# Performance work log

Hardware: AMD Instinct MI355X
Metric: run time of the kernel (lower is better)

The kernel has to match this reference:

```python
import jax, jax.numpy as jnp
import numpy as np

N_GRAPHS = 100
NODES_PER_GRAPH = 1000
N = N_GRAPHS * NODES_PER_GRAPH
DEG = 16
E = N * DEG
IN_FEATS = 64
HIDDEN = 128
READOUT_DIM = HIDDEN // 2
SLOPE = 0.01
EPS = 1e-5


def leaky(x):
    return jnp.where(x >= 0, x, SLOPE * x)


def _kaiming(k, shape):
    # torch kaiming_uniform_, fan_in mode, leaky_relu gain
    fan_in = shape[0]
    gain = np.sqrt(2.0 / (1.0 + SLOPE ** 2))
    bound = gain * np.sqrt(3.0 / fan_in)
    return jax.random.uniform(k, shape, jnp.float32, -bound, bound)


def setup_inputs() -> dict:
    key = jax.random.key(0)
    ks = jax.random.split(key, 16)
    node_feats = jax.random.normal(ks[0], (N, IN_FEATS), jnp.float32)
    # within-graph random edges (batched graph of equal-sized components)
    src_local = jax.random.randint(ks[1], (E,), 0, NODES_PER_GRAPH)
    dst_local = jax.random.randint(ks[2], (E,), 0, NODES_PER_GRAPH)
    edge_graph = jnp.repeat(jnp.arange(N_GRAPHS, dtype=jnp.int32), E // N_GRAPHS)
    src = (edge_graph * NODES_PER_GRAPH + src_local).astype(jnp.int32)
    dst = (edge_graph * NODES_PER_GRAPH + dst_local).astype(jnp.int32)
    edge_weights = jax.random.uniform(ks[3], (E,), jnp.float32)
    node_graph = jnp.repeat(jnp.arange(N_GRAPHS, dtype=jnp.int32), NODES_PER_GRAPH)
    return {
        "node_feats": node_feats,
        "edge_weights": edge_weights,
        "W1": _kaiming(ks[4], (IN_FEATS, HIDDEN)),
        "W2": _kaiming(ks[5], (HIDDEN, HIDDEN)),
        "gn1_alpha": jnp.ones((HIDDEN,), jnp.float32),
        "gn1_gamma": jnp.ones((HIDDEN,), jnp.float32),
        "gn1_beta": jnp.zeros((HIDDEN,), jnp.float32),
        "gn2_alpha": jnp.ones((HIDDEN,), jnp.float32),
        "gn2_gamma": jnp.ones((HIDDEN,), jnp.float32),
        "gn2_beta": jnp.zeros((HIDDEN,), jnp.float32),
        "r1_w1": _kaiming(ks[6], (HIDDEN, HIDDEN)),
        "r1_b1": jnp.zeros((HIDDEN,), jnp.float32),
        "r1_w2": _kaiming(ks[7], (HIDDEN, READOUT_DIM)),
        "r1_b2": jnp.zeros((READOUT_DIM,), jnp.float32),
        "r2_w1": _kaiming(ks[8], (HIDDEN, HIDDEN)),
        "r2_b1": jnp.zeros((HIDDEN,), jnp.float32),
        "r2_w2": _kaiming(ks[9], (HIDDEN, READOUT_DIM)),
        "r2_b2": jnp.zeros((READOUT_DIM,), jnp.float32),
        "src": src,
        "dst": dst,
        "node_graph": node_graph,
    }


def _graph_conv(x, W, src, dst, ew, out_isqrt, in_isqrt):
    # DGL GraphConv norm='both', no bias: D_in^{-1/2} A_w D_out^{-1/2} X W
    h = (x * out_isqrt[:, None]) @ W                 # [N, out]
    m = h[src] * ew[:, None]                         # [E, out] gather + edge weight
    agg = jax.ops.segment_sum(m, dst, num_segments=N)  # scatter-add
    return agg * in_isqrt[:, None]


def _graph_norm(x, alpha, gamma, beta, node_graph, inv_cnt):
    mean = jax.ops.segment_sum(x, node_graph, num_segments=N_GRAPHS) * inv_cnt
    sub = x - alpha * mean[node_graph]
    var = jax.ops.segment_sum(sub * sub, node_graph, num_segments=N_GRAPHS) * inv_cnt
    return gamma * sub / jnp.sqrt(var[node_graph] + EPS) + beta


def _readout(x, w1, b1, w2, b2, node_graph, inv_cnt):
    # deep-sets style universal readout: rho(mean(phi(h_v)))
    h = leaky(x @ w1 + b1)
    pooled = jax.ops.segment_sum(h, node_graph, num_segments=N_GRAPHS) * inv_cnt
    return leaky(pooled @ w2 + b2)


def reference(node_feats, edge_weights, W1, W2,
              gn1_alpha, gn1_gamma, gn1_beta,
              gn2_alpha, gn2_gamma, gn2_beta,
              r1_w1, r1_b1, r1_w2, r1_b2,
              r2_w1, r2_b1, r2_w2, r2_b2,
              src, dst, node_graph):
    ones_e = jnp.ones((E,), jnp.float32)
    out_deg = jnp.clip(jax.ops.segment_sum(ones_e, src, num_segments=N), 1.0)
    in_deg = jnp.clip(jax.ops.segment_sum(ones_e, dst, num_segments=N), 1.0)
    out_isqrt = jax.lax.rsqrt(out_deg)
    in_isqrt = jax.lax.rsqrt(in_deg)
    inv_cnt = 1.0 / NODES_PER_GRAPH

    h = _graph_conv(node_feats, W1, src, dst, edge_weights, out_isqrt, in_isqrt)
    h = leaky(_graph_norm(h, gn1_alpha, gn1_gamma, gn1_beta, node_graph, inv_cnt))
    # dropout is identity in eval mode
    r1 = _readout(h, r1_w1, r1_b1, r1_w2, r1_b2, node_graph, inv_cnt)
    m1 = jax.ops.segment_sum(h, node_graph, num_segments=N_GRAPHS) * inv_cnt

    h = _graph_conv(h, W2, src, dst, edge_weights, out_isqrt, in_isqrt)
    h = leaky(_graph_norm(h, gn2_alpha, gn2_gamma, gn2_beta, node_graph, inv_cnt))
    r2 = _readout(h, r2_w1, r2_b1, r2_w2, r2_b2, node_graph, inv_cnt)
    m2 = jax.ops.segment_sum(h, node_graph, num_segments=N_GRAPHS) * inv_cnt

    readout = jnp.concatenate([r1, m1, r2, m2], axis=1)  # [G, 2*H + 2*H/2] = [100, 384]
    return leaky(readout)
```

## Files before the change

### kernel.cpp

```cpp
#include <hip/hip_runtime.h>
#include <cstddef>
#include <cstdint>

#define NG   100
#define NPG  1000
#define NN   (NG * NPG)
#define NE   (NN * 16)
#define EPG  (NE / NG)
#define CSRL 24000
#define MINREC 20
#define FIN  64
#define HID  128
#define RD   64
#define SLOPE 0.01f
#define EPSV  1e-5f
#define NSTRIP 500
#define GSN   40

using short8 = __attribute__((ext_vector_type(8))) short;
using f32x4  = __attribute__((ext_vector_type(4))) float;
typedef unsigned short u16;

__device__ __forceinline__ float leaky(float x) { return x >= 0.f ? x : SLOPE * x; }

__device__ __forceinline__ u16 f2bf(float f) {
  union { float f; unsigned u; } v; v.f = f;
  return (u16)((v.u + 0x7fffu + ((v.u >> 16) & 1u)) >> 16);
}
__device__ __forceinline__ float bf2f(u16 u) {
  union { unsigned u; float f; } v; v.u = ((unsigned)u) << 16;
  return v.f;
}

__device__ __forceinline__ bool swz(int b, int per_g, int& g, int& part) {
  const int xcd = b & 7;
  const int slot = b >> 3;
  g = xcd + 8 * (slot / per_g);
  part = slot % per_g;
  return g < NG;
}

struct BldSh {
  unsigned csrl[CSRL];
  int hin[NPG];
  int hout[NPG];
  int cur[NPG];
  int wtot[16];
  int total;
};
struct GemSh { u16 Xl[64 * FIN]; u16 W[HID * FIN]; };
union FrontSh { BldSh b; GemSh g; };

__global__ __launch_bounds__(1024) void front_k(
    const float* __restrict__ X0, const float* __restrict__ ew,
    const int* __restrict__ src, const int* __restrict__ dst,
    const float* __restrict__ W1, const float* __restrict__ W2f,
    const float* __restrict__ R1f, const float* __restrict__ R2f,
    u16* __restrict__ Wt2, u16* __restrict__ Rt1, u16* __restrict__ Rt2,
    int* __restrict__ cin_, int* __restrict__ offs,
    unsigned* __restrict__ csr, u16* __restrict__ bufA,
    float* __restrict__ zeroreg) {
  __shared__ FrontSh u;
  const int b = blockIdx.x;
  const int t = threadIdx.x;
  if (b >= 208) {
    const int idx = (b - 208) * 1024 + t;
    {
      const int m = idx >> 14, r = idx & 16383;
      const int n = r >> 7, k = r & 127;
      const float* s = (m == 0) ? W2f : (m == 1) ? R1f : R2f;
      u16* d = (m == 0) ? Wt2 : (m == 1) ? Rt1 : Rt2;
      d[r] = f2bf(s[k * HID + n]);
    }
    if (idx < (8 * NG * HID) / 4)
      ((float4*)zeroreg)[idx] = make_float4(0.f, 0.f, 0.f, 0.f);
    return;
  }
  int g, part;
  if (!swz(b, 2, g, part)) return;
  const int lane = t & 63, wave = t >> 6;
  const int nb = g * NPG, eb = g * EPG;

  if (part == 0) {
    {
      const uint4 z4 = {0u, 0u, 0u, 0u};
      uint4* c4 = (uint4*)u.b.csrl;
#pragma unroll
      for (int i = 0; i < CSRL / 4 / 1024 + 1; ++i) {
        const int j = t + i * 1024;
        if (j < CSRL / 4) c4[j] = z4;
      }
    }
    if (t < NPG) { u.b.hin[t] = 0; u.b.hout[t] = 0; }
    __syncthreads();
    for (int e = t; e < EPG; e += 4096) {
      int s4[4], d4[4];
#pragma unroll
      for (int k = 0; k < 4; ++k) {
        const int ee = e + k * 1024;
        if (ee < EPG) { s4[k] = src[eb + ee]; d4[k] = dst[eb + ee]; }
        else d4[k] = -1;
      }
#pragma unroll
      for (int k = 0; k < 4; ++k)
        if (d4[k] >= 0) {
          atomicAdd(&u.b.hout[s4[k] - nb], 1);
          atomicAdd(&u.b.hin[d4[k] - nb], 1);
        }
    }
    __syncthreads();
    int v[4], vr[4];
    int loc = 0;
#pragma unroll
    for (int k = 0; k < 4; ++k) {
      const int idx = t * 4 + k;
      v[k] = (idx < NPG) ? u.b.hin[idx] : 0;
      const int c4 = (v[k] + 3) & ~3;
      vr[k] = (idx < NPG) ? ((c4 > MINREC) ? c4 : MINREC) : 0;
      loc += vr[k];
    }
    int incl = loc;
#pragma unroll
    for (int d = 1; d < 64; d <<= 1) {
      const int x = __shfl_up(incl, d);
      if (lane >= d) incl += x;
    }
    if (lane == 63) u.b.wtot[wave] = incl;
    if (t < NPG) cin_[nb + t] = u.b.hin[t];
    __syncthreads();
    float* houtf = (float*)u.b.hout;
    if (t < NPG) {
      const int c = u.b.hout[t];
      houtf[t] = rsqrtf((float)(c > 0 ? c : 1));
    }
    int wexc = 0;
    for (int i = 0; i < wave; ++i) wexc += u.b.wtot[i];
    int run = wexc + (incl - loc);
#pragma unroll
    for (int k = 0; k < 4; ++k) {
      const int idx = t * 4 + k;
      if (idx < NPG) {
        offs[nb + idx] = g * CSRL + run;
        u.b.cur[idx] = run;
        run += vr[k];
        if (idx == NPG - 1) u.b.total = run;
      }
    }
    __syncthreads();
    for (int e = t; e < EPG; e += 4096) {
      int s4[4], d4[4];
      float w4[4];
#pragma unroll
      for (int k = 0; k < 4; ++k) {
        const int ee = e + k * 1024;
        if (ee < EPG) { s4[k] = src[eb + ee]; d4[k] = dst[eb + ee]; w4[k] = ew[eb + ee]; }
        else d4[k] = -1;
      }
#pragma unroll
      for (int k = 0; k < 4; ++k)
        if (d4[k] >= 0) {
          const int sl = s4[k] - nb;
          const int pos = atomicAdd(&u.b.cur[d4[k] - nb], 1);
          if (pos < CSRL)
            u.b.csrl[pos] = ((unsigned)sl << 16) | (unsigned)f2bf(w4[k] * houtf[sl]);
        }
    }
    __syncthreads();
    {
      const int tot4 = (u.b.total + 3) >> 2;
      const uint4* s4p = (const uint4*)u.b.csrl;
      uint4* d4p = (uint4*)(csr + (size_t)g * CSRL);
      for (int i = t; i < tot4; i += 1024) d4p[i] = s4p[i];
    }
  } else {
    const int l15 = lane & 15, quad = lane >> 4;
    const int rg = wave >> 2, cg = wave & 3;
    {
      const int n = t & 127, ko = t >> 7;
      short8 w8;
#pragma unroll
      for (int j = 0; j < 8; ++j) w8[j] = (short)f2bf(W1[(ko * 8 + j) * HID + n]);
      *(short8*)&u.g.W[n * FIN + ((ko ^ (n & 7)) << 3)] = w8;
    }
    const int kq = t & 15, srow = t >> 4;
    float4 xpre = (srow < NPG)
        ? *(const float4*)(X0 + (size_t)(nb + srow) * FIN + kq * 4)
        : make_float4(0.f, 0.f, 0.f, 0.f);
    for (int pass = 0; pass < 16; ++pass) {
      __syncthreads();
      {
        ushort4 uu = make_ushort4(f2bf(xpre.x), f2bf(xpre.y), f2bf(xpre.z), f2bf(xpre.w));
        const int cc = kq >> 1, half = kq & 1;
        *(ushort4*)&u.g.Xl[srow * FIN + (((cc ^ (srow & 7)) << 3) | (half << 2))] = uu;
      }
      __syncthreads();
      if (pass < 15) {
        const int rowi = (pass + 1) * 64 + srow;
        xpre = (rowi < NPG)
            ? *(const float4*)(X0 + (size_t)(nb + rowi) * FIN + kq * 4)
            : make_float4(0.f, 0.f, 0.f, 0.f);
      }
      short8 a[2];
      const int arow = rg * 16 + l15;
#pragma unroll
      for (int kt = 0; kt < 2; ++kt)
        a[kt] = *(const short8*)&u.g.Xl[arow * FIN + (((kt * 4 + quad) ^ (l15 & 7)) << 3)];
      int rows[4];
#pragma unroll
      for (int r = 0; r < 4; ++r) rows[r] = pass * 64 + rg * 16 + quad * 4 + r;
#pragma unroll
      for (int q2 = 0; q2 < 2; ++q2) {
        const int ct = cg * 2 + q2;
        f32x4 acc = {0.f, 0.f, 0.f, 0.f};
        const int brow = ct * 16 + l15;
#pragma unroll
        for (int kt = 0; kt < 2; ++kt) {
          const short8 bb = *(const short8*)&u.g.W[brow * FIN + (((kt * 4 + quad) ^ (l15 & 7)) << 3)];
          acc = __builtin_amdgcn_mfma_f32_16x16x32_bf16(a[kt], bb, acc, 0, 0, 0);
        }
        const int n2 = ct * 16 + l15;
#pragma unroll
        for (int r = 0; r < 4; ++r)
          if (rows[r] < NPG)
            bufA[(size_t)(nb + rows[r]) * HID + n2] = f2bf(acc[r]);
      }
    }
  }
}

__device__ __forceinline__ void norm_affine(const float* sx, const float* sq,
                                            const float* alpha, const float* gamma,
                                            const float* beta, int g, int c8,
                                            float* Av, float* Bv) {
  const float inv = 1.0f / NPG;
#pragma unroll
  for (int j = 0; j < 8; ++j) {
    const int f = c8 * 8 + j;
    const float mean = sx[g * HID + f] * inv;
    const float ex2 = sq[g * HID + f] * inv;
    const float am = alpha[f] * mean;
    const float var = fmaxf(ex2 - 2.0f * am * mean + am * am, 0.0f);
    const float A = gamma[f] * rsqrtf(var + EPSV);
    Av[j] = A;
    Bv[j] = beta[f] - A * am;
  }
}

__global__ __launch_bounds__(256) void gather_k(const u16* __restrict__ H,
                                                const unsigned* __restrict__ csr,
                                                const int* __restrict__ offs,
                                                const int* __restrict__ cin_,
                                                u16* __restrict__ AGG,
                                                float* __restrict__ sx,
                                                float* __restrict__ sq) {
  __shared__ float redx[4][HID];
  __shared__ float redq[4][HID];
  const int wave = threadIdx.x >> 6;
  const int lane = threadIdx.x & 63;
  int g, part;
  if (!swz(blockIdx.x, 25, g, part)) return;
  const int nb = g * NPG;
  const int base = nb + part * GSN;
  const int loff = lane * 2;
  const u16* __restrict__ Hg = H + (size_t)nb * HID;

  float sxa = 0.f, sxb = 0.f, sqa = 0.f, sqb = 0.f;
  for (int it = 0; it < 3; ++it) {
    const int nc = (it < 2) ? 4 : 2;
    int nn[4], cnt[4], c4p[4];
    float isq[4];
    const uint4* p[4];
#pragma unroll
    for (int c = 0; c < 4; ++c) {
      const int j = it * 4 + c;
      const int node = base + wave + ((j < 10) ? j : 0) * 4;
      nn[c] = node;
      const int nu = __builtin_amdgcn_readfirstlane(node);
      const int off = __builtin_amdgcn_readfirstlane(offs[nu]);
      cnt[c] = (c < nc) ? __builtin_amdgcn_readfirstlane(cin_[nu]) : 0;
      const int cr = (cnt[c] + 3) & ~3;
      c4p[c] = ((cr > MINREC) ? cr : MINREC) >> 2;
      isq[c] = rsqrtf(fmaxf((float)cnt[c], 1.0f));
      p[c] = (const uint4*)__builtin_assume_aligned(csr + off, 16);
    }
    float ax[4] = {0.f, 0.f, 0.f, 0.f};
    float ay[4] = {0.f, 0.f, 0.f, 0.f};
#pragma unroll
    for (int t = 0; t < 5; ++t) {
      unsigned rs[4][4];
#pragma unroll
      for (int c = 0; c < 4; ++c)
        if (c < nc) {
          const uint4 rv = p[c][t];
          rs[c][0] = __builtin_amdgcn_readfirstlane(rv.x);
          rs[c][1] = __builtin_amdgcn_readfirstlane(rv.y);
          rs[c][2] = __builtin_amdgcn_readfirstlane(rv.z);
          rs[c][3] = __builtin_amdgcn_readfirstlane(rv.w);
        }
      unsigned uu[4][4];
#pragma unroll
      for (int c = 0; c < 4; ++c)
        if (c < nc) {
#pragma unroll
          for (int q = 0; q < 4; ++q)
            uu[c][q] = ((const unsigned*)(Hg + (size_t)(rs[c][q] >> 16) * HID))[lane];
        }
#pragma unroll
      for (int c = 0; c < 4; ++c)
        if (c < nc) {
#pragma unroll
          for (int q = 0; q < 4; ++q) {
            const float w = bf2f((u16)(rs[c][q] & 0xffffu));
            ax[c] = fmaf(w, __uint_as_float(uu[c][q] << 16), ax[c]);
            ay[c] = fmaf(w, __uint_as_float(uu[c][q] & 0xffff0000u), ay[c]);
          }
        }
    }
#pragma unroll
    for (int c = 0; c < 4; ++c) {
      for (int t = 5; t < c4p[c]; ++t) {
        const uint4 rv = p[c][t];
        unsigned rsd[4];
        rsd[0] = __builtin_amdgcn_readfirstlane(rv.x);
        rsd[1] = __builtin_amdgcn_readfirstlane(rv.y);
        rsd[2] = __builtin_amdgcn_readfirstlane(rv.z);
        rsd[3] = __builtin_amdgcn_readfirstlane(rv.w);
#pragma unroll
        for (int q = 0; q < 4; ++q) {
          const unsigned uq = ((const unsigned*)(Hg + (size_t)(rsd[q] >> 16) * HID))[lane];
          const float w = bf2f((u16)(rsd[q] & 0xffffu));
          ax[c] = fmaf(w, __uint_as_float(uq << 16), ax[c]);
          ay[c] = fmaf(w, __uint_as_float(uq & 0xffff0000u), ay[c]);
        }
      }
    }
#pragma unroll
    for (int c = 0; c < 4; ++c)
      if (c < nc) {
        const float rx = ax[c] * isq[c];
        const float ry = ay[c] * isq[c];
        *(unsigned*)(AGG + (size_t)nn[c] * HID + loff) =
            (unsigned)f2bf(rx) | ((unsigned)f2bf(ry) << 16);
        sxa += rx; sxb += ry;
        sqa += rx * rx; sqb += ry * ry;
      }
  }
  redx[wave][loff] = sxa; redx[wave][loff + 1] = sxb;
  redq[wave][loff] = sqa; redq[wave][loff + 1] = sqb;
  __syncthreads();
  const int tid = threadIdx.x;
  if (tid < HID) {
    unsafeAtomicAdd(&sx[g * HID + tid],
                    redx[0][tid] + redx[1][tid] + redx[2][tid] + redx[3][tid]);
  } else {
    const int t = tid - HID;
    unsafeAtomicAdd(&sq[g * HID + t],
                    redq[0][t] + redq[1][t] + redq[2][t] + redq[3][t]);
  }
}

struct RedT { float red[32][HID]; float hred[32][HID]; };
union ShT { u16 Xl[128 * HID]; RedT r; };

template <bool DO_GEMM>
__global__ __launch_bounds__(512) void phigemm_k(const u16* __restrict__ Xb,
                                                 u16* __restrict__ Y,
                                                 const u16* __restrict__ Wt,
                                                 const u16* __restrict__ Rt,
                                                 const float* __restrict__ sx,
                                                 const float* __restrict__ sq,
                                                 const float* __restrict__ alpha,
                                                 const float* __restrict__ gamma,
                                                 const float* __restrict__ beta,
                                                 const float* __restrict__ b1,
                                                 float* __restrict__ phi_sum,
                                                 float* __restrict__ h_sum) {
  __shared__ ShT sh;
  __shared__ u16 Rl[HID * HID];
  __shared__ u16 Wl[DO_GEMM ? HID * HID : 8];
  const int tid = threadIdx.x;
  const int wave = tid >> 6, lane = tid & 63, l15 = lane & 15, quad = lane >> 4;
  int g, part;
  if (!swz(blockIdx.x, 2, g, part)) return;
  const int base = g * NPG + part * NSTRIP;
  const int c8 = tid & 15;
  const int srow = tid >> 4;

  for (int i = tid; i < HID * (HID / 8); i += 512) {
    const int n = i >> 4, c = i & 15;
    const short8 r2 = *(const short8*)(Rt + n * HID + c * 8);
    *(short8*)&Rl[n * HID + ((c ^ (n & 15)) << 3)] = r2;
    if (DO_GEMM) {
      const short8 w = *(const short8*)(Wt + n * HID + c * 8);
      *(short8*)&Wl[n * HID + ((c ^ (n & 15)) << 3)] = w;
    }
  }
  float Av[8], Bv[8];
  norm_affine(sx, sq, alpha, gamma, beta, g, c8, Av, Bv);
  float bcol[8];
#pragma unroll
  for (int ct = 0; ct < 8; ++ct) bcol[ct] = b1[ct * 16 + l15];

  float pooled[8] = {0.f, 0.f, 0.f, 0.f, 0.f, 0.f, 0.f, 0.f};
  float hp[8] = {0.f, 0.f, 0.f, 0.f, 0.f, 0.f, 0.f, 0.f};
  const short8 z8 = {0, 0, 0, 0, 0, 0, 0, 0};
  short8 xpre[4];
#pragma unroll
  for (int it = 0; it < 4; ++it) {
    const int rowi = srow + it * 32;
    xpre[it] = (rowi < NSTRIP) ? *(const short8*)(Xb + (size_t)(base + rowi) * HID + c8 * 8) : z8;
  }
  for (int pass = 0; pass < 4; ++pass) {
    __syncthreads();
#pragma unroll
    for (int it = 0; it < 4; ++it) {
      const int r = srow + it * 32;
      const int rowi = pass * 128 + r;
      short8 o = z8;
      if (rowi < NSTRIP) {
#pragma unroll
        for (int j = 0; j < 8; ++j) {
          const float xn = leaky(fmaf(Av[j], bf2f((u16)xpre[it][j]), Bv[j]));
          hp[j] += xn;
          o[j] = (short)f2bf(xn);
        }
      }
      *(short8*)&sh.Xl[r * HID + ((c8 ^ (r & 15)) << 3)] = o;
    }
    __syncthreads();
    if (pass < 3) {
#pragma unroll
      for (int it = 0; it < 4; ++it) {
        const int rowi = (pass + 1) * 128 + srow + it * 32;
        xpre[it] = (rowi < NSTRIP) ? *(const short8*)(Xb + (size_t)(base + rowi) * HID + c8 * 8) : z8;
      }
    }
    short8 a[4];
    const int arow = wave * 16 + l15;
#pragma unroll
    for (int kt = 0; kt < 4; ++kt)
      a[kt] = *(const short8*)&sh.Xl[arow * HID + (((kt * 4 + quad) ^ l15) << 3)];
    int rows[4];
#pragma unroll
    for (int r = 0; r < 4; ++r) rows[r] = pass * 128 + wave * 16 + quad * 4 + r;
#pragma unroll
    for (int ct = 0; ct < 8; ++ct) {
      const int brow = ct * 16 + l15;
      if (DO_GEMM) {
        f32x4 accW = {0.f, 0.f, 0.f, 0.f};
#pragma unroll
        for (int kt = 0; kt < 4; ++kt) {
          const short8 bb = *(const short8*)&Wl[brow * HID + (((kt * 4 + quad) ^ l15) << 3)];
          accW = __builtin_amdgcn_mfma_f32_16x16x32_bf16(a[kt], bb, accW, 0, 0, 0);
        }
#pragma unroll
        for (int r = 0; r < 4; ++r)
          if (rows[r] < NSTRIP)
            Y[(size_t)(base + rows[r]) * HID + ct * 16 + l15] = f2bf(accW[r]);
      }
      f32x4 accR = {0.f, 0.f, 0.f, 0.f};
#pragma unroll
      for (int kt = 0; kt < 4; ++kt) {
        const short8 bb = *(const short8*)&Rl[brow * HID + (((kt * 4 + quad) ^ l15) << 3)];
        accR = __builtin_amdgcn_mfma_f32_16x16x32_bf16(a[kt], bb, accR, 0, 0, 0);
      }
#pragma unroll
      for (int r = 0; r < 4; ++r)
        if (rows[r] < NSTRIP) pooled[ct] += leaky(accR[r] + bcol[ct]);
    }
  }
  __syncthreads();
  const int qi = wave * 4 + quad;
#pragma unroll
  for (int ct = 0; ct < 8; ++ct) sh.r.red[qi][ct * 16 + l15] = pooled[ct];
#pragma unroll
  for (int j = 0; j < 8; ++j) sh.r.hred[tid >> 4][(tid & 15) * 8 + j] = hp[j];
  __syncthreads();
  if (tid < HID) {
    float s = 0.f;
#pragma unroll
    for (int q = 0; q < 32; ++q) s += sh.r.red[q][tid];
    unsafeAtomicAdd(&phi_sum[g * HID + tid], s);
  } else if (tid < 2 * HID) {
    const int t = tid - HID;
    float s = 0.f;
#pragma unroll
    for (int rr = 0; rr < 32; ++rr) s += sh.r.hred[rr][t];
    unsafeAtomicAdd(&h_sum[g * HID + t], s);
  }
}

__global__ __launch_bounds__(64) void fin_k(const float* __restrict__ ps1,
                                            const float* __restrict__ hs1,
                                            const float* __restrict__ ps2,
                                            const float* __restrict__ hs2,
                                            const float* __restrict__ r1w2,
                                            const float* __restrict__ r1b2,
                                            const float* __restrict__ r2w2,
                                            const float* __restrict__ r2b2,
                                            float* __restrict__ out) {
  const int gb = blockIdx.x;
  const bool L2 = gb >= NG;
  const int g = L2 ? gb - NG : gb;
  const float* ps = L2 ? ps2 : ps1;
  const float* hs = L2 ? hs2 : hs1;
  const float* w2 = L2 ? r2w2 : r1w2;
  const float* b2 = L2 ? r2b2 : r1b2;
  const int roff = L2 ? 192 : 0;
  const int moff = L2 ? 256 : 64;
  const int j = threadIdx.x;
  float acc = b2[j];
#pragma unroll 8
  for (int k = 0; k < HID; ++k)
    acc += (ps[g * HID + k] * (1.0f / NPG)) * w2[k * RD + j];
  out[g * 384 + roff + j] = leaky(leaky(acc));
  out[g * 384 + moff + j] = leaky(hs[g * HID + j] * (1.0f / NPG));
  out[g * 384 + moff + 64 + j] = leaky(hs[g * HID + 64 + j] * (1.0f / NPG));
}

extern "C" void kernel_launch(void* const* d_in, const int* in_sizes, int n_in,
                              void* d_out, int out_size, void* d_ws, size_t ws_size,
                              hipStream_t stream) {
  const float* node_feats = (const float*)d_in[0];
  const float* ew   = (const float*)d_in[1];
  const float* W1   = (const float*)d_in[2];
  const float* W2   = (const float*)d_in[3];
  const float* g1a  = (const float*)d_in[4];
  const float* g1g  = (const float*)d_in[5];
  const float* g1b  = (const float*)d_in[6];
  const float* g2a  = (const float*)d_in[7];
  const float* g2g  = (const float*)d_in[8];
  const float* g2b  = (const float*)d_in[9];
  const float* r1w1 = (const float*)d_in[10];
  const float* r1b1 = (const float*)d_in[11];
  const float* r1w2 = (const float*)d_in[12];
  const float* r1b2 = (const float*)d_in[13];
  const float* r2w1 = (const float*)d_in[14];
  const float* r2b1 = (const float*)d_in[15];
  const float* r2w2 = (const float*)d_in[16];
  const float* r2b2 = (const float*)d_in[17];
  const int* src = (const int*)d_in[18];
  const int* dst = (const int*)d_in[19];
  float* out = (float*)d_out;

  char* wsb = (char*)d_ws;
  float* ps1     = (float*)wsb;
  float* hs1     = ps1 + NG * HID;
  float* ps2     = hs1 + NG * HID;
  float* hs2     = ps2 + NG * HID;
  float* sx1     = hs2 + NG * HID;
  float* sq1     = sx1 + NG * HID;
  float* sx2     = sq1 + NG * HID;
  float* sq2     = sx2 + NG * HID;
  int*   cin     = (int*)(sq2 + NG * HID);
  int*   offs    = cin + NN;
  unsigned* csr  = (unsigned*)(offs + NN);
  u16*   Wt2     = (u16*)(csr + (size_t)NG * CSRL);
  u16*   Rt1     = Wt2 + HID * HID;
  u16*   Rt2     = Rt1 + HID * HID;
  u16*   bufA    = Rt2 + HID * HID;
  u16*   bufB    = bufA + (size_t)NN * HID;

  const int gemm_grid = 8 * 2 * 13;
  const int gather_grid = 8 * 25 * 13;

  front_k<<<256, 1024, 0, stream>>>(node_feats, ew, src, dst,
                                    W1, W2, r1w1, r2w1,
                                    Wt2, Rt1, Rt2,
                                    cin, offs, csr, bufA, ps1);

  gather_k<<<gather_grid, 256, 0, stream>>>(bufA, csr, offs, cin, bufB, sx1, sq1);
  phigemm_k<true><<<gemm_grid, 512, 0, stream>>>(bufB, bufA, Wt2, Rt1,
                                                 sx1, sq1, g1a, g1g, g1b,
                                                 r1b1, ps1, hs1);

  gather_k<<<gather_grid, 256, 0, stream>>>(bufA, csr, offs, cin, bufB, sx2, sq2);
  phigemm_k<false><<<gemm_grid, 512, 0, stream>>>(bufB, nullptr, nullptr, Rt2,
                                                  sx2, sq2, g2a, g2g, g2b,
                                                  r2b1, ps2, hs2);

  fin_k<<<2 * NG, 64, 0, stream>>>(ps1, hs1, ps2, hs2, r1w2, r1b2, r2w2, r2b2, out);
}
```

Baseline: 257.5 us.

## Split per-graph CSR build across two blocks by destination half

The per-graph CSR construction in the front kernel is now split across two blocks, each owning 500 destination nodes, with its own half-size shared CSR buffer and offset base. The grid grows to 3 parts per graph (two build, one GEMM) so build work runs in parallel and shared memory per block shrinks, which can improve occupancy. Each build block still scans all edges of the graph and recomputes the out-degree histogram, so edge loads and histogram work are duplicated.

```diff
diff --git a/kernel.cpp b/kernel.cpp
--- a/kernel.cpp
+++ b/kernel.cpp
@@ -8,6 +8,7 @@
 #define NE   (NN * 16)
 #define EPG  (NE / NG)
 #define CSRL 24000
+#define CSRH 12000
 #define MINREC 20
 #define FIN  64
 #define HID  128
@@ -41,11 +42,11 @@
 }
 
 struct BldSh {
-  unsigned csrl[CSRL];
-  int hin[NPG];
+  unsigned csrl[CSRH];
   int hout[NPG];
-  int cur[NPG];
-  int wtot[16];
+  int hin[NPG / 2];
+  int cur[NPG / 2];
+  int wtot[8];
   int total;
 };
 struct GemSh { u16 Xl[64 * FIN]; u16 W[HID * FIN]; };
@@ -63,8 +64,8 @@
   __shared__ FrontSh u;
   const int b = blockIdx.x;
   const int t = threadIdx.x;
-  if (b >= 208) {
-    const int idx = (b - 208) * 1024 + t;
+  if (b >= 312) {
+    const int idx = (b - 312) * 1024 + t;
     {
       const int m = idx >> 14, r = idx & 16383;
       const int n = r >> 7, k = r & 127;
@@ -77,21 +78,23 @@
     return;
   }
   int g, part;
-  if (!swz(b, 2, g, part)) return;
+  if (!swz(b, 3, g, part)) return;
   const int lane = t & 63, wave = t >> 6;
   const int nb = g * NPG, eb = g * EPG;
 
-  if (part == 0) {
+  if (part < 2) {
+    const int nbase = part * 500;
     {
       const uint4 z4 = {0u, 0u, 0u, 0u};
       uint4* c4 = (uint4*)u.b.csrl;
 #pragma unroll
-      for (int i = 0; i < CSRL / 4 / 1024 + 1; ++i) {
+      for (int i = 0; i < 3; ++i) {
         const int j = t + i * 1024;
-        if (j < CSRL / 4) c4[j] = z4;
-      }
-    }
-    if (t < NPG) { u.b.hin[t] = 0; u.b.hout[t] = 0; }
+        if (j < CSRH / 4) c4[j] = z4;
+      }
+    }
+    if (t < NPG) u.b.hout[t] = 0;
+    if (t < 500) u.b.hin[t] = 0;
     __syncthreads();
     for (int e = t; e < EPG; e += 4096) {
       int s4[4], d4[4];
@@ -105,46 +108,39 @@
       for (int k = 0; k < 4; ++k)
         if (d4[k] >= 0) {
           atomicAdd(&u.b.hout[s4[k] - nb], 1);
-          atomicAdd(&u.b.hin[d4[k] - nb], 1);
-        }
-    }
-    __syncthreads();
-    int v[4], vr[4];
-    int loc = 0;
-#pragma unroll
-    for (int k = 0; k < 4; ++k) {
-      const int idx = t * 4 + k;
-      v[k] = (idx < NPG) ? u.b.hin[idx] : 0;
-      const int c4 = (v[k] + 3) & ~3;
-      vr[k] = (idx < NPG) ? ((c4 > MINREC) ? c4 : MINREC) : 0;
-      loc += vr[k];
-    }
-    int incl = loc;
-#pragma unroll
-    for (int d = 1; d < 64; d <<= 1) {
-      const int x = __shfl_up(incl, d);
-      if (lane >= d) incl += x;
-    }
-    if (lane == 63) u.b.wtot[wave] = incl;
-    if (t < NPG) cin_[nb + t] = u.b.hin[t];
+          const int dl = d4[k] - nb - nbase;
+          if ((unsigned)dl < 500u) atomicAdd(&u.b.hin[dl], 1);
+        }
+    }
     __syncthreads();
     float* houtf = (float*)u.b.hout;
     if (t < NPG) {
       const int c = u.b.hout[t];
       houtf[t] = rsqrtf((float)(c > 0 ? c : 1));
     }
-    int wexc = 0;
-    for (int i = 0; i < wave; ++i) wexc += u.b.wtot[i];
-    int run = wexc + (incl - loc);
-#pragma unroll
-    for (int k = 0; k < 4; ++k) {
-      const int idx = t * 4 + k;
-      if (idx < NPG) {
-        offs[nb + idx] = g * CSRL + run;
-        u.b.cur[idx] = run;
-        run += vr[k];
-        if (idx == NPG - 1) u.b.total = run;
-      }
+    int v = 0, vr = 0;
+    int incl = 0;
+    if (t < 512) {
+      v = (t < 500) ? u.b.hin[t] : 0;
+      const int c4v = (v + 3) & ~3;
+      vr = (t < 500) ? ((c4v > MINREC) ? c4v : MINREC) : 0;
+      incl = vr;
+#pragma unroll
+      for (int d = 1; d < 64; d <<= 1) {
+        const int x = __shfl_up(incl, d);
+        if (lane >= d) incl += x;
+      }
+      if (lane == 63) u.b.wtot[wave] = incl;
+    }
+    if (t < 500) cin_[nb + nbase + t] = v;
+    __syncthreads();
+    if (t < 500) {
+      int wexc = 0;
+      for (int i = 0; i < wave; ++i) wexc += u.b.wtot[i];
+      const int run = wexc + incl - vr;
+      offs[nb + nbase + t] = g * CSRL + part * CSRH + run;
+      u.b.cur[t] = run;
+      if (t == 499) u.b.total = run + vr;
     }
     __syncthreads();
     for (int e = t; e < EPG; e += 4096) {
@@ -159,17 +155,20 @@
 #pragma unroll
       for (int k = 0; k < 4; ++k)
         if (d4[k] >= 0) {
-          const int sl = s4[k] - nb;
-          const int pos = atomicAdd(&u.b.cur[d4[k] - nb], 1);
-          if (pos < CSRL)
-            u.b.csrl[pos] = ((unsigned)sl << 16) | (unsigned)f2bf(w4[k] * houtf[sl]);
+          const int dl = d4[k] - nb - nbase;
+          if ((unsigned)dl < 500u) {
+            const int sl = s4[k] - nb;
+            const int pos = atomicAdd(&u.b.cur[dl], 1);
+            if (pos < CSRH)
+              u.b.csrl[pos] = ((unsigned)sl << 16) | (unsigned)f2bf(w4[k] * houtf[sl]);
+          }
         }
     }
     __syncthreads();
     {
       const int tot4 = (u.b.total + 3) >> 2;
       const uint4* s4p = (const uint4*)u.b.csrl;
-      uint4* d4p = (uint4*)(csr + (size_t)g * CSRL);
+      uint4* d4p = (uint4*)(csr + (size_t)g * CSRL + part * CSRH);
       for (int i = t; i < tot4; i += 1024) d4p[i] = s4p[i];
     }
   } else {
@@ -564,10 +563,10 @@
   const int gemm_grid = 8 * 2 * 13;
   const int gather_grid = 8 * 25 * 13;
 
-  front_k<<<256, 1024, 0, stream>>>(node_feats, ew, src, dst,
-                                    W1, W2, r1w1, r2w1,
-                                    Wt2, Rt1, Rt2,
-                                    cin, offs, csr, bufA, ps1);
+  front_k<<<312 + 48, 1024, 0, stream>>>(node_feats, ew, src, dst,
+                                         W1, W2, r1w1, r2w1,
+                                         Wt2, Rt1, Rt2,
+                                         cin, offs, csr, bufA, ps1);
 
   gather_k<<<gather_grid, 256, 0, stream>>>(bufA, csr, offs, cin, bufB, sx1, sq1);
   phigemm_k<true><<<gemm_grid, 512, 0, stream>>>(bufB, bufA, Wt2, Rt1,
```

Result: no change. 259.5 us (+0.8%).
